# Performance work log

Measured on AMD Instinct MI355X. Metric: run time of the kernel, lower is better.

## Reference

```python
import jax, jax.numpy as jnp
import numpy as np

B, N, D, H = 256, 164, 1024, 8
NK = 100          # keypoint block size (hardcoded 100 in the module)
DH = D // H       # 128


def setup_inputs() -> dict:
    key = jax.random.key(0)
    ks = jax.random.split(key, 10)
    x = jax.random.normal(ks[0], (B, N, D), jnp.float32)
    xian = jax.random.normal(ks[1], (B, NK, NK), jnp.float32)
    # mask: True = masked. Keep the first NK columns unmasked so the dynamic-MLP
    # block never sees -finfo.max values (matches sane usage; avoids overflow).
    mask_tail = jax.random.bernoulli(ks[2], 0.1, (B, N - NK))
    mask = jnp.concatenate([jnp.zeros((B, NK), bool), mask_tail], axis=1)
    Wqkv = jax.random.normal(ks[3], (D, 3 * D), jnp.float32) * 0.02
    W1 = jax.random.normal(ks[4], (NK, 50), jnp.float32) * 0.1
    b1 = jnp.zeros((50,), jnp.float32)
    W2 = jax.random.normal(ks[5], (50, NK), jnp.float32) * 0.1
    b2 = jnp.zeros((NK,), jnp.float32)
    Wout = jax.random.normal(ks[6], (D, D), jnp.float32) * 0.02
    bout = jnp.zeros((D,), jnp.float32)
    return {"x": x, "mask": mask, "xian": xian, "Wqkv": Wqkv,
            "W1": W1, "b1": b1, "W2": W2, "b2": b2,
            "Wout": Wout, "bout": bout}


def reference(x, mask, xian, Wqkv, W1, b1, W2, b2, Wout, bout):
    scale = D ** -0.5  # scale_with_head=False -> dim**-0.5
    qkv = x @ Wqkv                                   # [B,N,3D]
    q, k, v = jnp.split(qkv, 3, axis=-1)
    def heads(t):
        return t.reshape(B, N, H, DH).transpose(0, 2, 1, 3)  # b h n d
    q, k, v = heads(q), heads(k), heads(v)
    dots = jnp.einsum('bhid,bhjd->bhij', q, k) * scale       # [B,H,N,N]
    mask_value = -jnp.finfo(dots.dtype).max
    dots = jnp.where(mask[:, None, None, :], mask_value, dots)
    # dynamic correction on the keypoint block
    aq = dots[:, :, :NK, :NK]                                # [B,H,100,100]
    lv = jax.nn.relu(jax.nn.relu(jax.nn.relu(aq) @ W1 + b1) @ W2 + b2)
    xin = aq + xian[:, None, :, :] * lv
    dots = dots.at[:, :, :NK, :NK].set(xin)
    attn = jax.nn.softmax(dots, axis=-1)
    out = jnp.einsum('bhij,bhjd->bhid', attn, v)             # [B,H,N,DH]
    out = out.transpose(0, 2, 1, 3).reshape(B, N, D)
    return out @ Wout + bout
```

## Files before the change

### kernel.cpp

```cpp
#include <hip/hip_runtime.h>
#include <hip/hip_bf16.h>
#include <cstdint>
#include <cstddef>

typedef __bf16 bf16;
typedef __attribute__((ext_vector_type(8))) __bf16 bf16x8;
typedef __attribute__((ext_vector_type(2))) __bf16 bf16x2;
typedef __attribute__((ext_vector_type(4))) __bf16 bf16x4;
typedef __attribute__((ext_vector_type(4))) float f32x4;

#define DEVI __device__ __forceinline__

constexpr int Bb = 256, Nn = 164, NKk = 100;
constexpr int Mm = Bb * Nn;
constexpr int JP = 192;

DEVI void gl_lds16(const void* g, void* l) {
  __builtin_amdgcn_global_load_lds(
      (const __attribute__((address_space(1))) void*)g,
      (__attribute__((address_space(3))) void*)l, 16, 0, 0);
}

DEVI int sw16(int row, int kb) { return row * 128 + ((kb ^ (row & 7)) * 8); }
DEVI int sw8(int row, int kb)  { return row * 64 + ((kb ^ (row & 7)) * 8); }

DEVI void barrier_raw() {
  asm volatile("" ::: "memory");
  __builtin_amdgcn_s_barrier();
  asm volatile("" ::: "memory");
}
DEVI void vm0_barrier() {
  asm volatile("s_waitcnt vmcnt(0)" ::: "memory");
  __builtin_amdgcn_s_barrier();
  asm volatile("" ::: "memory");
}

__global__ void k_cvt_bf16(const float* __restrict__ in, bf16* __restrict__ out, int n) {
  int stride = gridDim.x * blockDim.x;
  for (int i = blockIdx.x * blockDim.x + threadIdx.x; i < (n >> 2); i += stride) {
    float4 v = ((const float4*)in)[i];
    bf16x4 o;
    o[0] = (bf16)v.x; o[1] = (bf16)v.y; o[2] = (bf16)v.z; o[3] = (bf16)v.w;
    ((bf16x4*)out)[i] = o;
  }
}

__global__ void k_maskdet(const unsigned char* __restrict__ m, int* __restrict__ mode) {
  __shared__ int sbyte, sodd;
  if (threadIdx.x == 0) { sbyte = 0; sodd = 0; }
  __syncthreads();
  for (int i = threadIdx.x; i < Mm; i += 256)
    if ((i & 3) && m[i]) sbyte = 1;
  __syncthreads();
  if (sbyte == 0) {
    const int* m32 = (const int*)m;
    for (int i = 1 + 2 * (int)threadIdx.x; i < Mm; i += 512)
      if (m32[i] != 0) sodd = 1;
  }
  __syncthreads();
  if (threadIdx.x == 0) *mode = sbyte ? 1 : (sodd ? 0 : 2);
}

__global__ void k_prep_w(const float* __restrict__ W1, const float* __restrict__ W2,
                         bf16* __restrict__ w1t, bf16* __restrict__ w2t) {
  int tid = threadIdx.x;
  int4 z = make_int4(0, 0, 0, 0);
  for (int i = tid; i < 1024; i += 256) ((int4*)w1t)[i] = z;
  for (int i = tid; i < 896;  i += 256) ((int4*)w2t)[i] = z;
  __syncthreads();
  for (int idx = tid; idx < 5000; idx += 256) {
    int k = idx / 50, c = idx % 50;
    w1t[sw16(c, k >> 3) + (k & 7)] = (bf16)W1[idx];
  }
  for (int idx = tid; idx < 5000; idx += 256) {
    int c = idx / 100, jp = idx % 100;
    w2t[sw8(jp, c >> 3) + (c & 7)] = (bf16)W2[idx];
  }
}

__global__ void k_maskbias(const void* __restrict__ maskp, const int* __restrict__ mode,
                           float* __restrict__ mb) {
  int b = blockIdx.x, col = threadIdx.x;
  int mmode = *mode;
  float v;
  if (col < NKk) v = 0.f;
  else if (col < 164) {
    int mi = b * 164 + col;
    long long m = (mmode == 1) ? (long long)((const unsigned char*)maskp)[mi]
                : (mmode == 0) ? (long long)((const int*)maskp)[mi]
                               : ((const long long*)maskp)[mi];
    v = m ? -__FLT_MAX__ : 0.f;
  } else v = -__FLT_MAX__;
  mb[b * 192 + col] = v;
}

__global__ void k_xianT(const float* __restrict__ xian, float* __restrict__ xT) {
  __shared__ float t[32][33];
  int b = blockIdx.y;
  int gt = blockIdx.x & 3, jt = blockIdx.x >> 2;
  int tx = threadIdx.x & 31, ty = threadIdx.x >> 5;
#pragma unroll
  for (int i = 0; i < 4; ++i) {
    int gi = gt * 32 + ty + i * 8, jp = jt * 32 + tx;
    t[ty + i * 8][tx] = (gi < 100 && jp < 100) ? xian[((size_t)b * 100 + gi) * 100 + jp] : 0.f;
  }
  __syncthreads();
#pragma unroll
  for (int i = 0; i < 4; ++i) {
    int jp = jt * 32 + ty + i * 8, gi = gt * 32 + tx;
    if (jp < 100 && gi < 112)
      xT[((size_t)b * 100 + jp) * 112 + gi] = t[tx][ty + i * 8];
  }
}

__global__ void k_transpose_cvt(const float* __restrict__ in, bf16* __restrict__ out,
                                int R, int C) {
  __shared__ float tile[32][33];
  int c0 = blockIdx.x * 32, r0 = blockIdx.y * 32;
  int tx = threadIdx.x & 31, ty = threadIdx.x >> 5;
#pragma unroll
  for (int i = 0; i < 4; ++i) {
    int r = ty + i * 8;
    tile[r][tx] = in[(size_t)(r0 + r) * C + c0 + tx];
  }
  __syncthreads();
#pragma unroll
  for (int i = 0; i < 4; ++i) {
    int rr = ty + i * 8;
    out[(size_t)(c0 + rr) * R + r0 + tx] = (bf16)tile[tx][rr];
  }
}

template <int MODE>
__global__ __launch_bounds__(512, 2) void k_gemm(const bf16* __restrict__ A,
                                                 const bf16* __restrict__ Bt,
                                                 void* __restrict__ Cout,
                                                 const float* __restrict__ bias,
                                                 bf16* __restrict__ vTout) {
  constexpr int K = 1024;
  constexpr int NT = 16;
  __shared__ __align__(16) char smem[131072];

  const int tid = threadIdx.x, lane = tid & 63, w = tid >> 6;
  const int l15 = lane & 15, l4 = lane >> 4;
  const int wm = w >> 2, wn = w & 3;

  const int nbx = (MODE == 0) ? 12 : 4;
  const int lin = blockIdx.x;
  const int cpx = gridDim.x >> 3;
  const int swz = (lin & 7) * cpx + (lin >> 3);
  const int tileM = (swz / nbx) * 256, tileN = (swz % nbx) * 256;

  size_t aoff[4], boff[4]; int loff[4];
#pragma unroll
  for (int li = 0; li < 4; ++li) {
    int idx = li * 512 + tid;
    int row = idx >> 3, sl = idx & 7;
    int kb = sl ^ (row & 7);
    aoff[li] = (size_t)(tileM + row) * K + kb * 8;
    boff[li] = (size_t)(tileN + row) * K + kb * 8;
    loff[li] = idx * 16;
  }

  f32x4 acc[8][4];
#pragma unroll
  for (int mf = 0; mf < 8; ++mf)
#pragma unroll
    for (int nf = 0; nf < 4; ++nf) acc[mf][nf] = f32x4{0.f, 0.f, 0.f, 0.f};

#pragma unroll
  for (int li = 0; li < 4; ++li) {
    gl_lds16(A + aoff[li], smem + loff[li]);
    gl_lds16(Bt + boff[li], smem + 65536 + loff[li]);
  }

  for (int t = 0; t < NT; ++t) {
    const int coff = (t & 1) << 15;
    const char* Ac = smem + coff;
    const char* Bc = smem + 65536 + coff;
    char* An = smem + (coff ^ 32768);
    char* Bn = smem + 65536 + (coff ^ 32768);
    const int kadd = (t + 1) * 64;
    const bool st = (t + 1) < NT;

    vm0_barrier();

    bf16x8 bfr[4][2];
#pragma unroll
    for (int nf = 0; nf < 4; ++nf) {
      int row = wn * 64 + nf * 16 + l15;
#pragma unroll
      for (int kk = 0; kk < 2; ++kk)
        bfr[nf][kk] = *(const bf16x8*)(Bc + row * 128 + (((kk * 4 + l4) ^ (row & 7)) * 16));
    }

#pragma unroll
    for (int ph = 0; ph < 4; ++ph) {
      if (st) {
        if (ph == 0) {
#pragma unroll
          for (int li = 0; li < 4; ++li)
            gl_lds16(A + aoff[li] + kadd, An + loff[li]);
        } else if (ph == 1) {
#pragma unroll
          for (int li = 0; li < 4; ++li)
            gl_lds16(Bt + boff[li] + kadd, Bn + loff[li]);
        }
      }
      bf16x8 af[2][2];
#pragma unroll
      for (int mi = 0; mi < 2; ++mi) {
        int row = wm * 128 + (ph * 2 + mi) * 16 + l15;
#pragma unroll
        for (int kk = 0; kk < 2; ++kk)
          af[mi][kk] = *(const bf16x8*)(Ac + row * 128 + (((kk * 4 + l4) ^ (row & 7)) * 16));
      }
      __builtin_amdgcn_s_setprio(1);
#pragma unroll
      for (int mi = 0; mi < 2; ++mi)
#pragma unroll
        for (int nf = 0; nf < 4; ++nf)
#pragma unroll
          for (int kk = 0; kk < 2; ++kk)
            acc[ph * 2 + mi][nf] = __builtin_amdgcn_mfma_f32_16x16x32_bf16(
                af[mi][kk], bfr[nf][kk], acc[ph * 2 + mi][nf], 0, 0, 0);
      __builtin_amdgcn_s_setprio(0);
      barrier_raw();
    }
  }

  if (MODE == 0 && tileN >= 2048) {
    const int h0 = (tileN - 2048) >> 7;
    bf16* Et = (bf16*)smem;
#pragma unroll
    for (int nh = 0; nh < 2; ++nh) {
      barrier_raw();
      if ((wn >> 1) == nh) {
#pragma unroll
        for (int mf = 0; mf < 8; ++mf)
#pragma unroll
          for (int nf = 0; nf < 4; ++nf) {
            int nr = (wn & 1) * 64 + nf * 16 + l15;
            int mr = wm * 128 + mf * 16 + l4 * 4;
            bf16x4 pv;
#pragma unroll
            for (int j = 0; j < 4; ++j) pv[j] = (bf16)acc[mf][nf][j];
            *(bf16x4*)&Et[nr * 264 + mr] = pv;
          }
      }
      barrier_raw();
#pragma unroll
      for (int r8 = 0; r8 < 8; ++r8) {
        int idx = r8 * 512 + tid;
        int nr = idx >> 5, m8 = (idx & 31) * 8;
        bf16x8 v = *(const bf16x8*)&Et[nr * 264 + m8];
        int m = tileM + m8;
        int b = m / 164, j = m - b * 164;
        if (j + 7 < 164) {
          size_t base = ((size_t)(b * 8 + h0 + nh) * 128 + nr) * JP + j;
          bf16x4 lo, hi;
#pragma unroll
          for (int e = 0; e < 4; ++e) { lo[e] = v[e]; hi[e] = v[e + 4]; }
          *(bf16x4*)&vTout[base] = lo;
          *(bf16x4*)&vTout[base + 4] = hi;
        } else {
#pragma unroll
          for (int e = 0; e < 8; ++e) {
            int me = m + e; int be = me / 164, je = me - be * 164;
            vTout[((size_t)(be * 8 + h0 + nh) * 128 + nr) * JP + je] = v[e];
          }
        }
      }
    }
  } else {
#pragma unroll
    for (int mf = 0; mf < 8; ++mf)
#pragma unroll
      for (int nf = 0; nf < 4; ++nf) {
        int m0 = tileM + wm * 128 + mf * 16 + l4 * 4;
        int n = tileN + wn * 64 + nf * 16 + l15;
        if (MODE == 0) {
#pragma unroll
          for (int j = 0; j < 4; ++j)
            ((bf16*)Cout)[(size_t)(m0 + j) * 3072 + n] = (bf16)acc[mf][nf][j];
        } else {
          float bv = bias[n];
#pragma unroll
          for (int j = 0; j < 4; ++j)
            ((float*)Cout)[(size_t)(m0 + j) * 1024 + n] = acc[mf][nf][j] + bv;
        }
      }
  }
}

__global__ __launch_bounds__(704, 3) void k_attn(
    const bf16* __restrict__ qkv, const bf16* __restrict__ vT,
    const bf16* __restrict__ w1t_g, const bf16* __restrict__ w2t_g,
    const float* __restrict__ maskbias, const float* __restrict__ xianT,
    const float* __restrict__ b1, const float* __restrict__ b2,
    bf16* __restrict__ aout) {
  __shared__ __align__(16) char smem[160448];
  bf16* VTs = (bf16*)smem;
  bf16* Ks  = (bf16*)(smem + 49152);
  bf16* AQs = (bf16*)(smem + 49152);
  bf16* Pw0 = (bf16*)(smem + 94208);
  bf16* W1T = (bf16*)(smem + 128000);
  bf16* H1s = (bf16*)(smem + 128000);
  bf16* W2T = (bf16*)(smem + 144384);
  float* biasL = (float*)(smem + 158720);
  float* b1L = (float*)(smem + 159744);
  float* b2L = (float*)(smem + 160000);

  const int tid = threadIdx.x, lane = tid & 63, w = tid >> 6;
  const int l15 = lane & 15, l4 = lane >> 4;
  const int i0 = blockIdx.x;
  const int bh = (i0 & 7) * 256 + (i0 >> 3);
  const int b = bh >> 3, h = bh & 7;
  const int rq = w * 16;
  const int pr12 = l15 % 12;

  bf16x8 qf[4];
  {
    int qrow = rq + l15; if (qrow > 163) qrow = 163;
    const bf16* qbase = qkv + (size_t)(b * 164 + qrow) * 3072 + h * 128;
#pragma unroll
    for (int kk = 0; kk < 4; ++kk)
      qf[kk] = *(const bf16x8*)(qbase + kk * 32 + l4 * 8);
  }

  for (int c = w; c < 41; c += 11) {
    int blk = c * 64 + lane;
    int r = blk >> 4, sl = blk & 15;
    int kb = sl ^ (r & 7);
    gl_lds16(qkv + (size_t)(b * 164 + r) * 3072 + 1024 + h * 128 + kb * 8, (char*)Ks + c * 1024);
  }
  if (w == 10 && lane < 48)
    gl_lds16(maskbias + b * 192 + lane * 4, (char*)biasL);
  if (tid < 192) {
    int r = 164 + (tid >> 4), sl = tid & 15;
    ((int4*)Ks)[r * 16 + sl] = make_int4(0, 0, 0, 0);
  }
  if (tid < 64) b1L[tid] = (tid < 50) ? b1[tid] : 0.f;
  else if (tid < 176) { int c = tid - 64; b2L[c] = (c < 100) ? b2[c] : 0.f; }
  __syncthreads();

  for (int c = w; c < 48; c += 11) {
    int blk = c * 64 + lane;
    int dh = blk / 24, sl = blk % 24;
    int kb = sl - (dh % 24); if (kb < 0) kb += 24;
    gl_lds16(vT + ((size_t)bh * 128 + dh) * JP + kb * 8, (char*)VTs + c * 1024);
  }
  for (int c = w; c < 16; c += 11)
    gl_lds16(w1t_g + c * 512 + lane * 8, (char*)W1T + c * 1024);
  for (int c = w; c < 14; c += 11)
    gl_lds16(w2t_g + c * 512 + lane * 8, (char*)W2T + c * 1024);

  constexpr float SC = 0.03125f;
  f32x4 s[11];
#pragma unroll
  for (int nt = 0; nt < 11; ++nt) {
    f32x4 acc = f32x4{0.f, 0.f, 0.f, 0.f};
#pragma unroll
    for (int kk = 0; kk < 4; ++kk) {
      bf16x8 kf = *(const bf16x8*)&Ks[sw16(nt * 16 + l15, kk * 4 + l4)];
      acc = __builtin_amdgcn_mfma_f32_16x16x32_bf16(kf, qf[kk], acc, 0, 0, 0);
    }
    f32x4 bv = *(const f32x4*)&biasL[nt * 16 + l4 * 4];
#pragma unroll
    for (int j = 0; j < 4; ++j) acc[j] = acc[j] * SC + bv[j];
    s[nt] = acc;
  }
  __syncthreads();

  if (w < 7) {
    int q = rq + l15;
#pragma unroll
    for (int nt = 0; nt < 8; ++nt) {
#pragma unroll
      for (int pr = 0; pr < 2; ++pr) {
        int k0 = nt * 16 + l4 * 4 + pr * 2;
        float v0 = (q < 100 && k0 < 100)     ? fmaxf(s[nt][pr * 2], 0.f)     : 0.f;
        float v1 = (q < 100 && k0 + 1 < 100) ? fmaxf(s[nt][pr * 2 + 1], 0.f) : 0.f;
        bf16x2 pv; pv[0] = (bf16)v0; pv[1] = (bf16)v1;
        *(bf16x2*)&AQs[sw16(q, k0 >> 3) + (k0 & 7)] = pv;
      }
    }
  }
  __syncthreads();

  f32x4 a1[3];
#pragma unroll
  for (int it = 0; it < 3; ++it) {
    int t = w + it * 11;
    f32x4 acc = f32x4{0.f, 0.f, 0.f, 0.f};
    if (t < 28) {
      int qs = t >> 2, ct = t & 3;
#pragma unroll
      for (int kk = 0; kk < 4; ++kk) {
        bf16x8 wf = *(const bf16x8*)&W1T[sw16(ct * 16 + l15, kk * 4 + l4)];
        bf16x8 af = *(const bf16x8*)&AQs[sw16(qs * 16 + l15, kk * 4 + l4)];
        acc = __builtin_amdgcn_mfma_f32_16x16x32_bf16(wf, af, acc, 0, 0, 0);
      }
    }
    a1[it] = acc;
  }
  __syncthreads();
#pragma unroll
  for (int it = 0; it < 3; ++it) {
    int t = w + it * 11;
    if (t < 28) {
      int qs = t >> 2, ct = t & 3;
      int qrow = qs * 16 + l15;
#pragma unroll
      for (int pr = 0; pr < 2; ++pr) {
        int c0 = ct * 16 + l4 * 4 + pr * 2;
        float v0 = (c0 < 50)     ? fmaxf(a1[it][pr * 2] + b1L[c0], 0.f)         : 0.f;
        float v1 = (c0 + 1 < 50) ? fmaxf(a1[it][pr * 2 + 1] + b1L[c0 + 1], 0.f) : 0.f;
        bf16x2 pv; pv[0] = (bf16)v0; pv[1] = (bf16)v1;
        *(bf16x2*)&H1s[sw8(qrow, c0 >> 3) + (c0 & 7)] = pv;
      }
    }
  }
  __syncthreads();

  if (w < 7) {
    int q = rq + l15;
#pragma unroll
    for (int nt2 = 0; nt2 < 7; ++nt2) {
      f32x4 acc = f32x4{0.f, 0.f, 0.f, 0.f};
#pragma unroll
      for (int kk = 0; kk < 2; ++kk) {
        bf16x8 wf = *(const bf16x8*)&W2T[sw8(nt2 * 16 + l15, kk * 4 + l4)];
        bf16x8 hf = *(const bf16x8*)&H1s[sw8(rq + l15, kk * 4 + l4)];
        acc = __builtin_amdgcn_mfma_f32_16x16x32_bf16(wf, hf, acc, 0, 0, 0);
      }
#pragma unroll
      for (int j = 0; j < 4; ++j) {
        int jp = nt2 * 16 + l4 * 4 + j;
        if (jp < 100 && q < 100) {
          float lv = fmaxf(acc[j] + b2L[jp], 0.f);
          s[nt2][j] += xianT[((size_t)b * 100 + jp) * 112 + q] * lv;
        }
      }
    }
  }

  float mx = -__FLT_MAX__;
#pragma unroll
  for (int nt = 0; nt < 11; ++nt)
#pragma unroll
    for (int j = 0; j < 4; ++j) mx = fmaxf(mx, s[nt][j]);
  mx = fmaxf(mx, __shfl_xor(mx, 16));
  mx = fmaxf(mx, __shfl_xor(mx, 32));
  float sum = 0.f;
#pragma unroll
  for (int nt = 0; nt < 11; ++nt)
#pragma unroll
    for (int j = 0; j < 4; ++j) { float e = __expf(s[nt][j] - mx); s[nt][j] = e; sum += e; }
  sum += __shfl_xor(sum, 16);
  sum += __shfl_xor(sum, 32);
  float rinv = 1.f / sum;

  bf16x2 pp[11][2];
#pragma unroll
  for (int nt = 0; nt < 11; ++nt)
#pragma unroll
    for (int pr = 0; pr < 2; ++pr) {
      bf16x2 pv;
      pv[0] = (bf16)(s[nt][pr * 2] * rinv);
      pv[1] = (bf16)(s[nt][pr * 2 + 1] * rinv);
      pp[nt][pr] = pv;
    }

  bf16* PwB = Pw0 + w * 1536;
  f32x4 o[8];
#pragma unroll
  for (int i = 0; i < 8; ++i) o[i] = f32x4{0.f, 0.f, 0.f, 0.f};
  int vmr[8];
#pragma unroll
  for (int i = 0; i < 8; ++i) vmr[i] = (i * 16 + l15) % 24;
#pragma unroll
  for (int hh = 0; hh < 2; ++hh) {
#pragma unroll
    for (int nn = 0; nn < 6; ++nn) {
      int nt = hh * 6 + nn;
      if (nt < 11) {
        int slot = nn * 2 + (l4 >> 1);
        int rs = slot + pr12; if (rs >= 12) rs -= 12;
#pragma unroll
        for (int pr = 0; pr < 2; ++pr)
          *(bf16x2*)&PwB[l15 * 96 + rs * 8 + (l4 & 1) * 4 + pr * 2] = pp[nt][pr];
      }
    }
#pragma unroll
    for (int kk2 = 0; kk2 < 3; ++kk2) {
      int rs = kk2 * 4 + l4 + pr12; if (rs >= 12) rs -= 12;
      bf16x8 af = *(const bf16x8*)&PwB[l15 * 96 + rs * 8];
#pragma unroll
      for (int i = 0; i < 8; ++i) {
        int sb = 12 * hh + kk2 * 4 + l4 + vmr[i]; if (sb >= 24) sb -= 24;
        bf16x8 bb = *(const bf16x8*)&VTs[(i * 16 + l15) * 192 + sb * 8];
        o[i] = __builtin_amdgcn_mfma_f32_16x16x32_bf16(af, bb, o[i], 0, 0, 0);
      }
    }
  }

#pragma unroll
  for (int i = 0; i < 8; ++i) {
    int dh = i * 16 + l15;
#pragma unroll
    for (int j = 0; j < 4; ++j) {
      int q = rq + l4 * 4 + j;
      if (q < 164)
        aout[(size_t)(b * 164 + q) * 1024 + h * 128 + dh] = (bf16)o[i][j];
    }
  }
}

extern "C" void kernel_launch(void* const* d_in, const int* in_sizes, int n_in,
                              void* d_out, int out_size, void* d_ws, size_t ws_size,
                              hipStream_t stream) {
  const float* x    = (const float*)d_in[0];
  const void* mask  = (const void*)d_in[1];
  const float* xian = (const float*)d_in[2];
  const float* Wqkv = (const float*)d_in[3];
  const float* W1   = (const float*)d_in[4];
  const float* b1   = (const float*)d_in[5];
  const float* W2   = (const float*)d_in[6];
  const float* b2   = (const float*)d_in[7];
  const float* Wout = (const float*)d_in[8];
  const float* bout = (const float*)d_in[9];
  float* out = (float*)d_out;
  char* ws = (char*)d_ws;

  bf16* xb    = (bf16*)(ws);
  bf16* wqkvT = (bf16*)(ws + 85983232ULL);
  bf16* woutT = (bf16*)(ws + 92274688ULL);
  bf16* qkvb  = (bf16*)(ws + 94371840ULL);
  bf16* vTb   = (bf16*)(ws + 352321536ULL);
  bf16* aoutb = (bf16*)(ws + 452984832ULL);
  int*   mmode    = (int*)(ws + 1024);
  bf16*  w1t_g    = (bf16*)(ws + 4096);
  bf16*  w2t_g    = (bf16*)(ws + 20480);
  float* maskbias = (float*)(ws + 36864);
  float* xianTp   = (float*)(ws + 262144);

  k_cvt_bf16<<<2048, 256, 0, stream>>>(x, xb, Mm * 1024);
  k_transpose_cvt<<<dim3(96, 32), 256, 0, stream>>>(Wqkv, wqkvT, 1024, 3072);
  k_transpose_cvt<<<dim3(32, 32), 256, 0, stream>>>(Wout, woutT, 1024, 1024);
  k_gemm<0><<<1968, 512, 0, stream>>>(xb, wqkvT, (void*)qkvb, nullptr, vTb);
  k_maskdet<<<1, 256, 0, stream>>>((const unsigned char*)mask, mmode);
  k_prep_w<<<1, 256, 0, stream>>>(W1, W2, w1t_g, w2t_g);
  k_maskbias<<<256, 192, 0, stream>>>(mask, mmode, maskbias);
  k_xianT<<<dim3(16, 256), 256, 0, stream>>>(xian, xianTp);
  k_attn<<<2048, 704, 0, stream>>>(qkvb, vTb, w1t_g, w2t_g, maskbias, xianTp,
                                   b1, b2, aoutb);
  k_gemm<1><<<656, 512, 0, stream>>>(aoutb, woutT, (void*)out, bout, nullptr);
}
```

Before: 736.2 us.

## Split dynamic-MLP correction into separate kernel to shrink attention LDS footprint

Moves the 100x100 keypoint-block MLP (relu(aq)@W1, relu @W2, times xian) out of the attention kernel into a new k_mlp kernel. That kernel recomputes the QK^T block and writes a fp32 delta tensor, which k_attn then adds to its scores. This removes the xian transpose kernel and cuts k_attn shared memory from about 160KB to about 95KB, which could allow more concurrent blocks per CU and drops several barriers. The cost is a second QK^T computation on the keypoint block and an extra global round-trip for the delta buffer, roughly 2048x100x112 floats. MLP weights are now read from global memory unswizzled instead of being staged in LDS.

```diff
diff --git a/kernel.cpp b/kernel.cpp
--- a/kernel.cpp
+++ b/kernel.cpp
@@ -70,11 +70,11 @@
   __syncthreads();
   for (int idx = tid; idx < 5000; idx += 256) {
     int k = idx / 50, c = idx % 50;
-    w1t[sw16(c, k >> 3) + (k & 7)] = (bf16)W1[idx];
+    w1t[c * 128 + k] = (bf16)W1[idx];
   }
   for (int idx = tid; idx < 5000; idx += 256) {
     int c = idx / 100, jp = idx % 100;
-    w2t[sw8(jp, c >> 3) + (c & 7)] = (bf16)W2[idx];
+    w2t[jp * 64 + c] = (bf16)W2[idx];
   }
 }
 
@@ -94,25 +94,6 @@
   mb[b * 192 + col] = v;
 }
 
-__global__ void k_xianT(const float* __restrict__ xian, float* __restrict__ xT) {
-  __shared__ float t[32][33];
-  int b = blockIdx.y;
-  int gt = blockIdx.x & 3, jt = blockIdx.x >> 2;
-  int tx = threadIdx.x & 31, ty = threadIdx.x >> 5;
-#pragma unroll
-  for (int i = 0; i < 4; ++i) {
-    int gi = gt * 32 + ty + i * 8, jp = jt * 32 + tx;
-    t[ty + i * 8][tx] = (gi < 100 && jp < 100) ? xian[((size_t)b * 100 + gi) * 100 + jp] : 0.f;
-  }
-  __syncthreads();
-#pragma unroll
-  for (int i = 0; i < 4; ++i) {
-    int jp = jt * 32 + ty + i * 8, gi = gt * 32 + tx;
-    if (jp < 100 && gi < 112)
-      xT[((size_t)b * 100 + jp) * 112 + gi] = t[tx][ty + i * 8];
-  }
-}
-
 __global__ void k_transpose_cvt(const float* __restrict__ in, bf16* __restrict__ out,
                                 int R, int C) {
   __shared__ float tile[32][33];
@@ -293,23 +274,134 @@
   }
 }
 
+__global__ __launch_bounds__(448) void k_mlp(
+    const bf16* __restrict__ qkv, const bf16* __restrict__ w1t_p,
+    const bf16* __restrict__ w2t_p, const float* __restrict__ xian,
+    const float* __restrict__ b1, const float* __restrict__ b2,
+    float* __restrict__ delta) {
+  __shared__ __align__(16) char smem[43008];
+  bf16* Ks  = (bf16*)smem;
+  bf16* AQs = (bf16*)smem;
+  bf16* H1s = (bf16*)(smem + 28672);
+
+  const int tid = threadIdx.x, lane = tid & 63, w = tid >> 6;
+  const int l15 = lane & 15, l4 = lane >> 4;
+  const int i0 = blockIdx.x;
+  const int bh = (i0 & 7) * 256 + (i0 >> 3);
+  const int b = bh >> 3, h = bh & 7;
+  const int q = w * 16 + l15;
+
+  for (int c = w; c < 25; c += 7) {
+    int blk = c * 64 + lane;
+    int r = blk >> 4, sl = blk & 15;
+    int kb = sl ^ (r & 7);
+    gl_lds16(qkv + (size_t)(b * 164 + r) * 3072 + 1024 + h * 128 + kb * 8, (char*)Ks + c * 1024);
+  }
+  if (tid < 192) {
+    int r = 100 + (tid >> 4), sl = tid & 15;
+    ((int4*)Ks)[r * 16 + sl] = make_int4(0, 0, 0, 0);
+  }
+  bf16x8 qf[4];
+  {
+    const bf16* qbase = qkv + (size_t)(b * 164 + q) * 3072 + h * 128;
+#pragma unroll
+    for (int kk = 0; kk < 4; ++kk)
+      qf[kk] = *(const bf16x8*)(qbase + kk * 32 + l4 * 8);
+  }
+  __syncthreads();
+
+  constexpr float SC = 0.03125f;
+  f32x4 s[7];
+#pragma unroll
+  for (int nt = 0; nt < 7; ++nt) {
+    f32x4 acc = f32x4{0.f, 0.f, 0.f, 0.f};
+#pragma unroll
+    for (int kk = 0; kk < 4; ++kk) {
+      bf16x8 kf = *(const bf16x8*)&Ks[sw16(nt * 16 + l15, kk * 4 + l4)];
+      acc = __builtin_amdgcn_mfma_f32_16x16x32_bf16(kf, qf[kk], acc, 0, 0, 0);
+    }
+#pragma unroll
+    for (int j = 0; j < 4; ++j) acc[j] *= SC;
+    s[nt] = acc;
+  }
+  __syncthreads();
+
+#pragma unroll
+  for (int nt = 0; nt < 8; ++nt) {
+#pragma unroll
+    for (int pr = 0; pr < 2; ++pr) {
+      int k0 = nt * 16 + l4 * 4 + pr * 2;
+      float v0 = (nt < 7 && q < 100 && k0 < 100)     ? fmaxf(s[nt][pr * 2], 0.f)     : 0.f;
+      float v1 = (nt < 7 && q < 100 && k0 + 1 < 100) ? fmaxf(s[nt][pr * 2 + 1], 0.f) : 0.f;
+      bf16x2 pv; pv[0] = (bf16)v0; pv[1] = (bf16)v1;
+      *(bf16x2*)&AQs[sw16(q, k0 >> 3) + (k0 & 7)] = pv;
+    }
+  }
+  __syncthreads();
+
+  f32x4 a1[4];
+#pragma unroll
+  for (int it = 0; it < 4; ++it) {
+    int t = w + it * 7;
+    int qs = t >> 2, ct = t & 3;
+    f32x4 acc = f32x4{0.f, 0.f, 0.f, 0.f};
+#pragma unroll
+    for (int kk = 0; kk < 4; ++kk) {
+      bf16x8 wf = *(const bf16x8*)(w1t_p + (ct * 16 + l15) * 128 + (kk * 4 + l4) * 8);
+      bf16x8 af = *(const bf16x8*)&AQs[sw16(qs * 16 + l15, kk * 4 + l4)];
+      acc = __builtin_amdgcn_mfma_f32_16x16x32_bf16(wf, af, acc, 0, 0, 0);
+    }
+    a1[it] = acc;
+  }
+#pragma unroll
+  for (int it = 0; it < 4; ++it) {
+    int t = w + it * 7;
+    int qs = t >> 2, ct = t & 3;
+    int qrow = qs * 16 + l15;
+#pragma unroll
+    for (int pr = 0; pr < 2; ++pr) {
+      int c0 = ct * 16 + l4 * 4 + pr * 2;
+      float v0 = (c0 < 50)     ? fmaxf(a1[it][pr * 2] + b1[c0], 0.f)         : 0.f;
+      float v1 = (c0 + 1 < 50) ? fmaxf(a1[it][pr * 2 + 1] + b1[c0 + 1], 0.f) : 0.f;
+      bf16x2 pv; pv[0] = (bf16)v0; pv[1] = (bf16)v1;
+      *(bf16x2*)&H1s[sw8(qrow, c0 >> 3) + (c0 & 7)] = pv;
+    }
+  }
+  __syncthreads();
+
+#pragma unroll
+  for (int nt2 = 0; nt2 < 7; ++nt2) {
+    f32x4 acc = f32x4{0.f, 0.f, 0.f, 0.f};
+#pragma unroll
+    for (int kk = 0; kk < 2; ++kk) {
+      bf16x8 wf = *(const bf16x8*)(w2t_p + (nt2 * 16 + l15) * 64 + (kk * 4 + l4) * 8);
+      bf16x8 hf = *(const bf16x8*)&H1s[sw8(q, kk * 4 + l4)];
+      acc = __builtin_amdgcn_mfma_f32_16x16x32_bf16(wf, hf, acc, 0, 0, 0);
+    }
+    if (q < 100) {
+      int jp0 = nt2 * 16 + l4 * 4;
+      f32x4 dv;
+#pragma unroll
+      for (int j = 0; j < 4; ++j) {
+        int jp = jp0 + j;
+        dv[j] = (jp < 100)
+              ? xian[((size_t)b * 100 + q) * 100 + jp] * fmaxf(acc[j] + b2[jp], 0.f)
+              : 0.f;
+      }
+      *(f32x4*)&delta[((size_t)bh * 100 + q) * 112 + jp0] = dv;
+    }
+  }
+}
+
 __global__ __launch_bounds__(704, 3) void k_attn(
     const bf16* __restrict__ qkv, const bf16* __restrict__ vT,
-    const bf16* __restrict__ w1t_g, const bf16* __restrict__ w2t_g,
-    const float* __restrict__ maskbias, const float* __restrict__ xianT,
-    const float* __restrict__ b1, const float* __restrict__ b2,
+    const float* __restrict__ maskbias, const float* __restrict__ delta,
     bf16* __restrict__ aout) {
-  __shared__ __align__(16) char smem[160448];
+  __shared__ __align__(16) char smem[94976];
   bf16* VTs = (bf16*)smem;
   bf16* Ks  = (bf16*)(smem + 49152);
-  bf16* AQs = (bf16*)(smem + 49152);
-  bf16* Pw0 = (bf16*)(smem + 94208);
-  bf16* W1T = (bf16*)(smem + 128000);
-  bf16* H1s = (bf16*)(smem + 128000);
-  bf16* W2T = (bf16*)(smem + 144384);
-  float* biasL = (float*)(smem + 158720);
-  float* b1L = (float*)(smem + 159744);
-  float* b2L = (float*)(smem + 160000);
+  bf16* Pw0 = (bf16*)(smem + 49152);
+  float* biasL = (float*)(smem + 94208);
 
   const int tid = threadIdx.x, lane = tid & 63, w = tid >> 6;
   const int l15 = lane & 15, l4 = lane >> 4;
@@ -318,10 +410,11 @@
   const int b = bh >> 3, h = bh & 7;
   const int rq = w * 16;
   const int pr12 = l15 % 12;
+  const int q = rq + l15;
 
   bf16x8 qf[4];
   {
-    int qrow = rq + l15; if (qrow > 163) qrow = 163;
+    int qrow = q; if (qrow > 163) qrow = 163;
     const bf16* qbase = qkv + (size_t)(b * 164 + qrow) * 3072 + h * 128;
 #pragma unroll
     for (int kk = 0; kk < 4; ++kk)
@@ -340,20 +433,23 @@
     int r = 164 + (tid >> 4), sl = tid & 15;
     ((int4*)Ks)[r * 16 + sl] = make_int4(0, 0, 0, 0);
   }
-  if (tid < 64) b1L[tid] = (tid < 50) ? b1[tid] : 0.f;
-  else if (tid < 176) { int c = tid - 64; b2L[c] = (c < 100) ? b2[c] : 0.f; }
-  __syncthreads();
-
+  __syncthreads();
+
+  f32x4 dv[7];
+  const bool hasd = (w < 7) && (q < 100);
+#pragma unroll
+  for (int nt = 0; nt < 7; ++nt) {
+    if (hasd)
+      dv[nt] = *(const f32x4*)&delta[((size_t)bh * 100 + q) * 112 + nt * 16 + l4 * 4];
+    else
+      dv[nt] = f32x4{0.f, 0.f, 0.f, 0.f};
+  }
   for (int c = w; c < 48; c += 11) {
     int blk = c * 64 + lane;
     int dh = blk / 24, sl = blk % 24;
     int kb = sl - (dh % 24); if (kb < 0) kb += 24;
     gl_lds16(vT + ((size_t)bh * 128 + dh) * JP + kb * 8, (char*)VTs + c * 1024);
   }
-  for (int c = w; c < 16; c += 11)
-    gl_lds16(w1t_g + c * 512 + lane * 8, (char*)W1T + c * 1024);
-  for (int c = w; c < 14; c += 11)
-    gl_lds16(w2t_g + c * 512 + lane * 8, (char*)W2T + c * 1024);
 
   constexpr float SC = 0.03125f;
   f32x4 s[11];
@@ -370,80 +466,11 @@
     for (int j = 0; j < 4; ++j) acc[j] = acc[j] * SC + bv[j];
     s[nt] = acc;
   }
-  __syncthreads();
-
-  if (w < 7) {
-    int q = rq + l15;
-#pragma unroll
-    for (int nt = 0; nt < 8; ++nt) {
-#pragma unroll
-      for (int pr = 0; pr < 2; ++pr) {
-        int k0 = nt * 16 + l4 * 4 + pr * 2;
-        float v0 = (q < 100 && k0 < 100)     ? fmaxf(s[nt][pr * 2], 0.f)     : 0.f;
-        float v1 = (q < 100 && k0 + 1 < 100) ? fmaxf(s[nt][pr * 2 + 1], 0.f) : 0.f;
-        bf16x2 pv; pv[0] = (bf16)v0; pv[1] = (bf16)v1;
-        *(bf16x2*)&AQs[sw16(q, k0 >> 3) + (k0 & 7)] = pv;
-      }
-    }
-  }
-  __syncthreads();
-
-  f32x4 a1[3];
-#pragma unroll
-  for (int it = 0; it < 3; ++it) {
-    int t = w + it * 11;
-    f32x4 acc = f32x4{0.f, 0.f, 0.f, 0.f};
-    if (t < 28) {
-      int qs = t >> 2, ct = t & 3;
-#pragma unroll
-      for (int kk = 0; kk < 4; ++kk) {
-        bf16x8 wf = *(const bf16x8*)&W1T[sw16(ct * 16 + l15, kk * 4 + l4)];
-        bf16x8 af = *(const bf16x8*)&AQs[sw16(qs * 16 + l15, kk * 4 + l4)];
-        acc = __builtin_amdgcn_mfma_f32_16x16x32_bf16(wf, af, acc, 0, 0, 0);
-      }
-    }
-    a1[it] = acc;
-  }
-  __syncthreads();
-#pragma unroll
-  for (int it = 0; it < 3; ++it) {
-    int t = w + it * 11;
-    if (t < 28) {
-      int qs = t >> 2, ct = t & 3;
-      int qrow = qs * 16 + l15;
-#pragma unroll
-      for (int pr = 0; pr < 2; ++pr) {
-        int c0 = ct * 16 + l4 * 4 + pr * 2;
-        float v0 = (c0 < 50)     ? fmaxf(a1[it][pr * 2] + b1L[c0], 0.f)         : 0.f;
-        float v1 = (c0 + 1 < 50) ? fmaxf(a1[it][pr * 2 + 1] + b1L[c0 + 1], 0.f) : 0.f;
-        bf16x2 pv; pv[0] = (bf16)v0; pv[1] = (bf16)v1;
-        *(bf16x2*)&H1s[sw8(qrow, c0 >> 3) + (c0 & 7)] = pv;
-      }
-    }
-  }
-  __syncthreads();
-
-  if (w < 7) {
-    int q = rq + l15;
-#pragma unroll
-    for (int nt2 = 0; nt2 < 7; ++nt2) {
-      f32x4 acc = f32x4{0.f, 0.f, 0.f, 0.f};
-#pragma unroll
-      for (int kk = 0; kk < 2; ++kk) {
-        bf16x8 wf = *(const bf16x8*)&W2T[sw8(nt2 * 16 + l15, kk * 4 + l4)];
-        bf16x8 hf = *(const bf16x8*)&H1s[sw8(rq + l15, kk * 4 + l4)];
-        acc = __builtin_amdgcn_mfma_f32_16x16x32_bf16(wf, hf, acc, 0, 0, 0);
-      }
-#pragma unroll
-      for (int j = 0; j < 4; ++j) {
-        int jp = nt2 * 16 + l4 * 4 + j;
-        if (jp < 100 && q < 100) {
-          float lv = fmaxf(acc[j] + b2L[jp], 0.f);
-          s[nt2][j] += xianT[((size_t)b * 100 + jp) * 112 + q] * lv;
-        }
-      }
-    }
-  }
+
+#pragma unroll
+  for (int nt = 0; nt < 7; ++nt)
+#pragma unroll
+    for (int j = 0; j < 4; ++j) s[nt][j] += dv[nt][j];
 
   float mx = -__FLT_MAX__;
 #pragma unroll
@@ -471,6 +498,7 @@
       pv[1] = (bf16)(s[nt][pr * 2 + 1] * rinv);
       pp[nt][pr] = pv;
     }
+  __syncthreads();
 
   bf16* PwB = Pw0 + w * 1536;
   f32x4 o[8];
@@ -510,9 +538,9 @@
     int dh = i * 16 + l15;
 #pragma unroll
     for (int j = 0; j < 4; ++j) {
-      int q = rq + l4 * 4 + j;
-      if (q < 164)
-        aout[(size_t)(b * 164 + q) * 1024 + h * 128 + dh] = (bf16)o[i][j];
+      int qq = rq + l4 * 4 + j;
+      if (qq < 164)
+        aout[(size_t)(b * 164 + qq) * 1024 + h * 128 + dh] = (bf16)o[i][j];
     }
   }
 }
@@ -543,7 +571,7 @@
   bf16*  w1t_g    = (bf16*)(ws + 4096);
   bf16*  w2t_g    = (bf16*)(ws + 20480);
   float* maskbias = (float*)(ws + 36864);
-  float* xianTp   = (float*)(ws + 262144);
+  float* deltap   = (float*)(ws + 262144);
 
   k_cvt_bf16<<<2048, 256, 0, stream>>>(x, xb, Mm * 1024);
   k_transpose_cvt<<<dim3(96, 32), 256, 0, stream>>>(Wqkv, wqkvT, 1024, 3072);
@@ -552,8 +580,7 @@
   k_maskdet<<<1, 256, 0, stream>>>((const unsigned char*)mask, mmode);
   k_prep_w<<<1, 256, 0, stream>>>(W1, W2, w1t_g, w2t_g);
   k_maskbias<<<256, 192, 0, stream>>>(mask, mmode, maskbias);
-  k_xianT<<<dim3(16, 256), 256, 0, stream>>>(xian, xianTp);
-  k_attn<<<2048, 704, 0, stream>>>(qkvb, vTb, w1t_g, w2t_g, maskbias, xianTp,
-                                   b1, b2, aoutb);
+  k_mlp<<<2048, 448, 0, stream>>>(qkvb, w1t_g, w2t_g, xian, b1, b2, deltap);
+  k_attn<<<2048, 704, 0, stream>>>(qkvb, vTb, maskbias, deltap, aoutb);
   k_gemm<1><<<656, 512, 0, stream>>>(aoutb, woutT, (void*)out, bout, nullptr);
 }
```

After: 762.5 us. 3.6% more time.
